# Performance work log

Measured on AMD Instinct MI355X. Metric: run time of the kernel, lower is better.

## Reference

```python
import jax, jax.numpy as jnp
import numpy as np

L = 64       # num_steps
NHID = 256   # nhid
N = 64       # cache_N
TOPK = 8     # cache_k


def setup_inputs() -> dict:
    key = jax.random.key(0)
    k1, k2, k3 = jax.random.split(key, 3)
    query = jax.random.normal(k1, (1, L, 32, NHID), dtype=jnp.float32)
    keys = jax.random.normal(k2, (N, 32, L * NHID), dtype=jnp.float32)       # stacked key_i buffers
    values = jax.random.normal(k3, (N, L, 32, 4 * NHID), dtype=jnp.float32)  # stacked value_i buffers, (nlayers+1)*nhid=1024
    return {"query": query, "keys": keys, "values": values}


def reference(query, keys, values):
    # query: (query_len=1, L, bsz, nhid) -> transpose(1,2) -> (1, bsz, L, nhid)
    q = jnp.swapaxes(query, 1, 2)
    qlen, bsz = q.shape[0], q.shape[1]
    q = q.reshape(qlen, bsz, -1)                 # no_summary: (1, bsz, dk)
    keys_t = jnp.swapaxes(keys, 0, 1)            # (bsz, N, dk)
    _vals = jnp.einsum('klbh->bklh', values)     # (bsz, N, L, h); computed in original, unused in max_pooling branch
    # max_pooling branch
    q2 = q.reshape(-1, L, NHID)                  # (bsz, L, nhid)
    pk = keys_t.reshape(-1, N, L, NHID)          # (bsz, N, L, nhid)
    att = jnp.einsum('bih,bnjh->bijn', q2, pk)   # (bsz, L, L, N)
    att = att.reshape(-1, L * L, 1, N).max(axis=1)  # (bsz, 1, N) max-pool over all step pairs
    att = att.reshape(-1, 1, N)
    _, topk_idx = jax.lax.top_k(att, TOPK)       # (bsz, 1, topk)
    topk_idx = jnp.squeeze(topk_idx, axis=1).T   # (topk, bsz)
    return att, topk_idx
```

## Files before the change

kernel.cpp:

```cpp
#include <hip/hip_runtime.h>
#include <hip/hip_bf16.h>
#include <math.h>

namespace {

constexpr int L   = 64;
constexpr int NH  = 256;
constexpr int NC  = 64;
constexpr int BSZ = 32;

typedef float f32x4 __attribute__((ext_vector_type(4)));
typedef short bf16x8 __attribute__((ext_vector_type(8)));

__device__ inline void split8(const float4 x0, const float4 x1,
                              bf16x8& hi, bf16x8& lo) {
  float f[8];
  *(float4*)(f)     = x0;
  *(float4*)(f + 4) = x1;
#pragma unroll
  for (int q = 0; q < 8; ++q) {
    const __hip_bfloat16 h = __float2bfloat16(f[q]);
    unsigned short hu;
    __builtin_memcpy(&hu, &h, 2);
    const float hf = __builtin_bit_cast(float, (unsigned)hu << 16);
    const __hip_bfloat16 l = __float2bfloat16(f[q] - hf);
    unsigned short lu;
    __builtin_memcpy(&lu, &l, 2);
    hi[q] = (short)hu;
    lo[q] = (short)lu;
  }
}

__device__ inline void gl16(const void* g, void* l) {
  __builtin_amdgcn_global_load_lds(
      (const __attribute__((address_space(1))) unsigned*)(g),
      (__attribute__((address_space(3))) unsigned*)(l), 16, 0, 0);
}


__global__ __launch_bounds__(256) void qsplit_kernel(
    const float* __restrict__ query, char* __restrict__ ws) {
  const int X = blockIdx.x;
  const int b = X >> 3;
  const int s = (X & 7) * 256 + threadIdx.x;
  const int it = s >> 9;
  const int kc = (s >> 6) & 7;
  const int l  = s & 63;
  const int row = it * 16 + (l & 15);
  const int col = kc * 32 + ((l >> 4) & 3) * 4;
  const float* src = query + ((size_t)row * BSZ + b) * NH + col;
  bf16x8 hi, lo;
  split8(*(const float4*)src, *(const float4*)(src + 16), hi, lo);
  char* wb = ws + (size_t)b * 65536;
  *(bf16x8*)(wb + (size_t)s * 16)         = hi;
  *(bf16x8*)(wb + 32768 + (size_t)s * 16) = lo;
}

__global__ __launch_bounds__(512, 4) void attmax_mfma(
    const float* __restrict__ keys,
    const char* __restrict__ ws,
    float* __restrict__ out)
{
  __shared__ __align__(16) char qlds[64 * 1024];
  __shared__ float wm[8];
  const short* Qhi = (const short*)qlds;
  const short* Qlo = (const short*)(qlds + 32768);

  const unsigned X = blockIdx.x;
  const int b  = X & 31;
  const int ng = X >> 5;

  const int tid  = threadIdx.x;
  const int w    = tid >> 6;
  const int lane = tid & 63;
  const int n     = ng * 4 + (w >> 1);
  const int jhalf = w & 1;

  {
    const char* src = ws + (size_t)b * 65536;
#pragma unroll
    for (int q = 0; q < 8; ++q) {
      const int off = (q * 8 + w) * 1024;
      gl16(src + off + lane * 16, qlds + off);
    }
  }
  __syncthreads();

  const float* kb = keys + ((size_t)n * BSZ + b) * (size_t)(L * NH)
                  + (size_t)jhalf * 32 * NH;
  const int rl = lane & 15;
  const int cq = ((lane >> 4) & 3) * 4;
  const float* kp0 = kb + (size_t)rl * NH + cq;
  const float* kp1 = kb + (size_t)(16 + rl) * NH + cq;

  f32x4 acc[4][2];
#pragma unroll
  for (int it = 0; it < 4; ++it)
#pragma unroll
    for (int jt = 0; jt < 2; ++jt)
#pragma unroll
      for (int e = 0; e < 4; ++e) acc[it][jt][e] = 0.f;

  float4 K0[4], K1[4];

#define LOADC(B, kc)                                     \
  do {                                                   \
    const float* p = kp0 + (kc) * 32;                    \
    (B)[0] = *(const float4*)(p);                        \
    (B)[1] = *(const float4*)(p + 16);                   \
    const float* q = kp1 + (kc) * 32;                    \
    (B)[2] = *(const float4*)(q);                        \
    (B)[3] = *(const float4*)(q + 16);                   \
  } while (0)

#define COMPC(B, kc)                                                          \
  do {                                                                        \
    bf16x8 bh0, bl0, bh1, bl1;                                                \
    split8((B)[0], (B)[1], bh0, bl0);                                         \
    split8((B)[2], (B)[3], bh1, bl1);                                         \
    _Pragma("unroll")                                                         \
    for (int it = 0; it < 4; ++it) {                                          \
      const int slot = ((it * 8 + (kc)) * 64 + lane) * 8;                     \
      const bf16x8 ah = *(const bf16x8*)&Qhi[slot];                           \
      const bf16x8 al = *(const bf16x8*)&Qlo[slot];                           \
      acc[it][0] = __builtin_amdgcn_mfma_f32_16x16x32_bf16(al, bh0, acc[it][0], 0, 0, 0); \
      acc[it][0] = __builtin_amdgcn_mfma_f32_16x16x32_bf16(ah, bl0, acc[it][0], 0, 0, 0); \
      acc[it][0] = __builtin_amdgcn_mfma_f32_16x16x32_bf16(ah, bh0, acc[it][0], 0, 0, 0); \
      acc[it][1] = __builtin_amdgcn_mfma_f32_16x16x32_bf16(al, bh1, acc[it][1], 0, 0, 0); \
      acc[it][1] = __builtin_amdgcn_mfma_f32_16x16x32_bf16(ah, bl1, acc[it][1], 0, 0, 0); \
      acc[it][1] = __builtin_amdgcn_mfma_f32_16x16x32_bf16(ah, bh1, acc[it][1], 0, 0, 0); \
    }                                                                         \
  } while (0)

  LOADC(K0, 0); LOADC(K1, 1);
  COMPC(K0, 0); LOADC(K0, 2);
  COMPC(K1, 1); LOADC(K1, 3);
  COMPC(K0, 2); LOADC(K0, 4);
  COMPC(K1, 3); LOADC(K1, 5);
  COMPC(K0, 4); LOADC(K0, 6);
  COMPC(K1, 5); LOADC(K1, 7);
  COMPC(K0, 6);
  COMPC(K1, 7);
#undef LOADC
#undef COMPC

  float m = -INFINITY;
#pragma unroll
  for (int it = 0; it < 4; ++it)
#pragma unroll
    for (int jt = 0; jt < 2; ++jt)
#pragma unroll
      for (int e = 0; e < 4; ++e) m = fmaxf(m, acc[it][jt][e]);
#pragma unroll
  for (int off = 1; off < 64; off <<= 1)
    m = fmaxf(m, __shfl_xor(m, off, 64));

  if (lane == 0) wm[w] = m;
  __syncthreads();
  if (lane == 0 && (w & 1) == 0)
    out[(size_t)b * NC + n] = fmaxf(wm[w], wm[w + 1]);
}

__global__ __launch_bounds__(64) void topk_kernel(float* __restrict__ out) {
  const int b = blockIdx.x;
  const int l = threadIdx.x;
  float v = out[b * NC + l];
#pragma unroll
  for (int k = 0; k < 8; ++k) {
    float bv = v;
    int bi = l;
#pragma unroll
    for (int off = 1; off < 64; off <<= 1) {
      const float ov = __shfl_xor(bv, off, 64);
      const int oi = __shfl_xor(bi, off, 64);
      if (ov > bv || (ov == bv && oi < bi)) { bv = ov; bi = oi; }
    }
    if (l == 0) out[BSZ * NC + k * BSZ + b] = (float)bi;
    if (l == bi) v = -INFINITY;
  }
}

}

extern "C" void kernel_launch(void* const* d_in, const int* in_sizes, int n_in,
                              void* d_out, int out_size, void* d_ws, size_t ws_size,
                              hipStream_t stream) {
  const float* query = (const float*)d_in[0];
  const float* keys  = (const float*)d_in[1];
  float* out = (float*)d_out;
  char*  ws  = (char*)d_ws;

  qsplit_kernel<<<dim3(256), dim3(256), 0, stream>>>(query, ws);
  attmax_mfma<<<dim3(512), dim3(512), 0, stream>>>(keys, ws, out);
  topk_kernel<<<dim3(BSZ), dim3(64), 0, stream>>>(out);
}
```

Baseline: 40.82 us.

## Stage keys tile in LDS with swizzle, keep query fragments in registers

Restructures the attention-max kernel so each block handles one (batch, cache entry) pair with 4 waves. The full 64KB key tile is streamed into LDS through async global-to-LDS loads with an XOR swizzle, and each wave keeps its 16-row query hi/lo fragments in registers. The previous version staged query in LDS and loaded keys directly into registers. The goal is fully coalesced, bulk key loads and more blocks in flight (2048 instead of 512), at the cost of no overlap between the load and compute phases within a block, and higher register pressure.

Measured after the change: 43.28 us. +6.0%, slower.

```diff
diff --git a/kernel.cpp b/kernel.cpp
--- a/kernel.cpp
+++ b/kernel.cpp
@@ -56,109 +56,85 @@
   *(bf16x8*)(wb + 32768 + (size_t)s * 16) = lo;
 }
 
-__global__ __launch_bounds__(512, 4) void attmax_mfma(
+__global__ __launch_bounds__(256, 2) void attmax_mfma(
     const float* __restrict__ keys,
     const char* __restrict__ ws,
     float* __restrict__ out)
 {
-  __shared__ __align__(16) char qlds[64 * 1024];
-  __shared__ float wm[8];
-  const short* Qhi = (const short*)qlds;
-  const short* Qlo = (const short*)(qlds + 32768);
+  __shared__ __align__(16) char klds[64 * 1024];
+  __shared__ float wm[4];
 
   const unsigned X = blockIdx.x;
-  const int b  = X & 31;
-  const int ng = X >> 5;
+  const int b = X & 31;
+  const int n = X >> 5;
 
   const int tid  = threadIdx.x;
   const int w    = tid >> 6;
   const int lane = tid & 63;
-  const int n     = ng * 4 + (w >> 1);
-  const int jhalf = w & 1;
 
+  const float* kb = keys + ((size_t)n * BSZ + b) * (size_t)(L * NH);
+
+#pragma unroll
+  for (int jj = 0; jj < 16; ++jj) {
+    const int j = w * 16 + jj;
+    const char* src = (const char*)(kb + (size_t)j * NH) + ((lane ^ (j & 7)) * 16);
+    gl16(src, klds + j * 1024);
+  }
+
+  bf16x8 ah[8], al[8];
   {
-    const char* src = ws + (size_t)b * 65536;
+    const char* wb = ws + (size_t)b * 65536;
 #pragma unroll
-    for (int q = 0; q < 8; ++q) {
-      const int off = (q * 8 + w) * 1024;
-      gl16(src + off + lane * 16, qlds + off);
+    for (int kc = 0; kc < 8; ++kc) {
+      const int slot = ((w * 8 + kc) * 64 + lane) * 16;
+      ah[kc] = *(const bf16x8*)(wb + slot);
+      al[kc] = *(const bf16x8*)(wb + 32768 + slot);
     }
   }
+
+  asm volatile("s_waitcnt vmcnt(0)" ::: "memory");
+  __builtin_amdgcn_sched_barrier(0);
   __syncthreads();
 
-  const float* kb = keys + ((size_t)n * BSZ + b) * (size_t)(L * NH)
-                  + (size_t)jhalf * 32 * NH;
   const int rl = lane & 15;
-  const int cq = ((lane >> 4) & 3) * 4;
-  const float* kp0 = kb + (size_t)rl * NH + cq;
-  const float* kp1 = kb + (size_t)(16 + rl) * NH + cq;
+  const int q4 = ((lane >> 4) & 3);
+  const int sw = lane & 7;
 
-  f32x4 acc[4][2];
+  f32x4 acc[4];
 #pragma unroll
-  for (int it = 0; it < 4; ++it)
+  for (int jt = 0; jt < 4; ++jt)
 #pragma unroll
-    for (int jt = 0; jt < 2; ++jt)
+    for (int e = 0; e < 4; ++e) acc[jt][e] = 0.f;
+
 #pragma unroll
-      for (int e = 0; e < 4; ++e) acc[it][jt][e] = 0.f;
-
-  float4 K0[4], K1[4];
-
-#define LOADC(B, kc)                                     \
-  do {                                                   \
-    const float* p = kp0 + (kc) * 32;                    \
-    (B)[0] = *(const float4*)(p);                        \
-    (B)[1] = *(const float4*)(p + 16);                   \
-    const float* q = kp1 + (kc) * 32;                    \
-    (B)[2] = *(const float4*)(q);                        \
-    (B)[3] = *(const float4*)(q + 16);                   \
-  } while (0)
-
-#define COMPC(B, kc)                                                          \
-  do {                                                                        \
-    bf16x8 bh0, bl0, bh1, bl1;                                                \
-    split8((B)[0], (B)[1], bh0, bl0);                                         \
-    split8((B)[2], (B)[3], bh1, bl1);                                         \
-    _Pragma("unroll")                                                         \
-    for (int it = 0; it < 4; ++it) {                                          \
-      const int slot = ((it * 8 + (kc)) * 64 + lane) * 8;                     \
-      const bf16x8 ah = *(const bf16x8*)&Qhi[slot];                           \
-      const bf16x8 al = *(const bf16x8*)&Qlo[slot];                           \
-      acc[it][0] = __builtin_amdgcn_mfma_f32_16x16x32_bf16(al, bh0, acc[it][0], 0, 0, 0); \
-      acc[it][0] = __builtin_amdgcn_mfma_f32_16x16x32_bf16(ah, bl0, acc[it][0], 0, 0, 0); \
-      acc[it][0] = __builtin_amdgcn_mfma_f32_16x16x32_bf16(ah, bh0, acc[it][0], 0, 0, 0); \
-      acc[it][1] = __builtin_amdgcn_mfma_f32_16x16x32_bf16(al, bh1, acc[it][1], 0, 0, 0); \
-      acc[it][1] = __builtin_amdgcn_mfma_f32_16x16x32_bf16(ah, bl1, acc[it][1], 0, 0, 0); \
-      acc[it][1] = __builtin_amdgcn_mfma_f32_16x16x32_bf16(ah, bh1, acc[it][1], 0, 0, 0); \
-    }                                                                         \
-  } while (0)
-
-  LOADC(K0, 0); LOADC(K1, 1);
-  COMPC(K0, 0); LOADC(K0, 2);
-  COMPC(K1, 1); LOADC(K1, 3);
-  COMPC(K0, 2); LOADC(K0, 4);
-  COMPC(K1, 3); LOADC(K1, 5);
-  COMPC(K0, 4); LOADC(K0, 6);
-  COMPC(K1, 5); LOADC(K1, 7);
-  COMPC(K0, 6);
-  COMPC(K1, 7);
-#undef LOADC
-#undef COMPC
+  for (int jt = 0; jt < 4; ++jt) {
+    const char* rowb = klds + (jt * 16 + rl) * 1024;
+#pragma unroll
+    for (int kc = 0; kc < 8; ++kc) {
+      const float4 x0 = *(const float4*)(rowb + (((kc * 8 + q4) ^ sw) * 16));
+      const float4 x1 = *(const float4*)(rowb + (((kc * 8 + 4 + q4) ^ sw) * 16));
+      bf16x8 bh, bl;
+      split8(x0, x1, bh, bl);
+      acc[jt] = __builtin_amdgcn_mfma_f32_16x16x32_bf16(al[kc], bh, acc[jt], 0, 0, 0);
+      acc[jt] = __builtin_amdgcn_mfma_f32_16x16x32_bf16(ah[kc], bl, acc[jt], 0, 0, 0);
+      acc[jt] = __builtin_amdgcn_mfma_f32_16x16x32_bf16(ah[kc], bh, acc[jt], 0, 0, 0);
+    }
+  }
 
   float m = -INFINITY;
 #pragma unroll
-  for (int it = 0; it < 4; ++it)
+  for (int jt = 0; jt < 4; ++jt)
 #pragma unroll
-    for (int jt = 0; jt < 2; ++jt)
-#pragma unroll
-      for (int e = 0; e < 4; ++e) m = fmaxf(m, acc[it][jt][e]);
+    for (int e = 0; e < 4; ++e) m = fmaxf(m, acc[jt][e]);
 #pragma unroll
   for (int off = 1; off < 64; off <<= 1)
     m = fmaxf(m, __shfl_xor(m, off, 64));
 
   if (lane == 0) wm[w] = m;
   __syncthreads();
-  if (lane == 0 && (w & 1) == 0)
-    out[(size_t)b * NC + n] = fmaxf(wm[w], wm[w + 1]);
+  if (tid == 0)
+    out[(size_t)b * NC + n] =
+        fmaxf(fmaxf(wm[0], wm[1]), fmaxf(wm[2], wm[3]));
 }
 
 __global__ __launch_bounds__(64) void topk_kernel(float* __restrict__ out) {
@@ -191,6 +167,6 @@
   char*  ws  = (char*)d_ws;
 
   qsplit_kernel<<<dim3(256), dim3(256), 0, stream>>>(query, ws);
-  attmax_mfma<<<dim3(512), dim3(512), 0, stream>>>(keys, ws, out);
+  attmax_mfma<<<dim3(2048), dim3(256), 0, stream>>>(keys, ws, out);
   topk_kernel<<<dim3(BSZ), dim3(64), 0, stream>>>(out);
 }
```
